# Optimization experiments

Measured on AMD Instinct MI355X. Metric: run time of the kernel, lower is better.

## Reference

```python
import jax, jax.numpy as jnp
import numpy as np


def setup_inputs() -> dict:
    key = jax.random.key(0)
    k1, k2 = jax.random.split(key)
    N, P, SMK, L = 256, 64, 2048, 32
    inp = jax.random.normal(k1, (N, P, SMK, 2), dtype=jnp.float32)
    # channel taps; in the original these are randn scaled by sqrt(power/2)
    cof = jax.random.normal(k2, (N, P, L, 2), dtype=jnp.float32) * 0.1
    return {"input": inp, "cof": cof, "M": 64}


def reference(input, cof, M):
    # input: (N, P, SMK, 2) real/imag stacked; cof: (N, P, L, 2)
    N, P, SMK, _ = input.shape
    L = cof.shape[2]
    sig = (input[..., 0] + 1j * input[..., 1]).reshape(N * P, SMK)   # complex64
    h = (cof[..., 0] + 1j * cof[..., 1]).reshape(N * P, L)
    # torch path: conv1d with time-reversed taps and padding=L-1 == FULL linear
    # convolution; four real convs == one complex conv.
    out_c = jax.vmap(lambda s, k: jnp.convolve(s, k, mode="full"))(sig, h)  # (N*P, SMK+L-1)
    output = jnp.stack([out_c.real, out_c.imag], axis=-1).reshape(N, P, SMK + L - 1, 2)
    # H_t = FFT of zero-padded taps along the tap axis (length M)
    cof_zp = jnp.pad(cof, ((0, 0), (0, 0), (0, M - L), (0, 0)))
    Hc = jnp.fft.fft(cof_zp[..., 0] + 1j * cof_zp[..., 1], axis=-1)  # (N, P, M)
    H_t = jnp.stack([Hc.real, Hc.imag], axis=-1)                      # (N, P, M, 2)
    return output, H_t
```

## Files before the change

kernel.cpp:

```cpp
#include <hip/hip_runtime.h>
#include <math.h>

#define SMK    2048
#define TAPS   32
#define OUTLEN (SMK + TAPS - 1)
#define PAD    32
#define SLOTS  (PAD + SMK + PAD)
#define NF4    (SLOTS / 2)
#define MDFT   64

typedef float v2f __attribute__((ext_vector_type(2)));

__device__ __forceinline__ float rfl(float x) {
    return __int_as_float(__builtin_amdgcn_readfirstlane(__float_as_int(x)));
}

__global__ __launch_bounds__(256, 8)
void conv_kernel(const float* __restrict__ input,
                 const float* __restrict__ cof,
                 float* __restrict__ out0,
                 float* __restrict__ out1)
{
    __shared__ float4 S4[NF4];
    __shared__ float2 s_tw[MDFT];

    const int tid = threadIdx.x;
    const int row = blockIdx.x;

    const float4* gin = (const float4*)(input + (size_t)row * (SMK * 2));
    #pragma unroll
    for (int k = 0; k < 4; ++k) S4[16 + tid + 256 * k] = gin[tid + 256 * k];
    if (tid < 16) {
        S4[tid] = make_float4(0.f, 0.f, 0.f, 0.f);
    } else if (tid < 32) {
        S4[1024 + tid] = make_float4(0.f, 0.f, 0.f, 0.f);
    }
    if (tid >= 64 && tid < 128) {
        int j = tid - 64;
        float sv, cv;
        __sincosf(-2.0f * (float)M_PI * (float)j / (float)MDFT, &sv, &cv);
        s_tw[j] = make_float2(cv, sv);
    }

    const float2* __restrict__ ct = (const float2*)(cof + (size_t)row * (TAPS * 2));
    float hre[TAPS], him[TAPS];
    #pragma unroll
    for (int l = 0; l < TAPS; ++l) {
        float2 tv = ct[l];
        hre[l] = rfl(tv.x);
        him[l] = rfl(tv.y);
    }
    __syncthreads();

    float2* go2 = (float2*)(out0 + (size_t)row * (OUTLEN * 2));

    #pragma unroll 1
    for (int j = 0; j < 2; ++j) {
        const int tf = 4 * tid + 1 + 1024 * j;

        v2f accA[4], accB[4];
        #pragma unroll
        for (int k = 0; k < 4; ++k) { accA[k] = (v2f)(0.f); accB[k] = (v2f)(0.f); }

        #pragma unroll
        for (int c = 0; c < 4; ++c) {
            const int base4 = 2 * tid + 512 * j - 4 * c + 13;
            float4 w4[6];
            #pragma unroll
            for (int i = 0; i < 6; ++i) w4[i] = S4[base4 + i];

            #pragma unroll
            for (int lp = 0; lp < 8; ++lp) {
                const int l = 8 * c + lp;
                const v2f hv = { hre[l], him[l] };
                #pragma unroll
                for (int k = 0; k < 4; ++k) {
                    const int q = k - lp + 7;
                    const float sx = (q & 1) ? w4[q >> 1].z : w4[q >> 1].x;
                    const float sy = (q & 1) ? w4[q >> 1].w : w4[q >> 1].y;
                    accA[k] = __builtin_elementwise_fma((v2f){ sx, sx }, hv, accA[k]);
                    accB[k] = __builtin_elementwise_fma((v2f){ sy, sy }, hv, accB[k]);
                }
            }
            __builtin_amdgcn_sched_barrier(0);
        }

        #pragma unroll
        for (int k = 0; k < 4; ++k)
            go2[tf + k] = make_float2(accA[k].x - accB[k].y, accA[k].y + accB[k].x);
    }

    const float2* S2 = (const float2*)S4;

    if (tid < MDFT) {
        const int kk = tid;
        v2f aA = (v2f)(0.f), aB = (v2f)(0.f);
        #pragma unroll
        for (int l = 0; l < TAPS; ++l) {
            const v2f hv = { hre[l], him[l] };
            float2 w = s_tw[(kk * l) & (MDFT - 1)];
            aA = __builtin_elementwise_fma((v2f){ w.x, w.x }, hv, aA);
            aB = __builtin_elementwise_fma((v2f){ w.y, w.y }, hv, aB);
        }
        ((float2*)out1)[(size_t)row * MDFT + kk] =
            make_float2(aA.x - aB.y, aA.y + aB.x);
    }
    else if (tid >= 128 && tid <= 158) {
        const int t = (tid == 158) ? 0 : (2049 + (tid - 128));
        v2f aA = (v2f)(0.f), aB = (v2f)(0.f);
        #pragma unroll
        for (int l = 0; l < TAPS; ++l) {
            const v2f hv = { hre[l], him[l] };
            float2 s = S2[PAD + t - l];
            aA = __builtin_elementwise_fma((v2f){ s.x, s.x }, hv, aA);
            aB = __builtin_elementwise_fma((v2f){ s.y, s.y }, hv, aB);
        }
        go2[t] = make_float2(aA.x - aB.y, aA.y + aB.x);
    }
}

extern "C" void kernel_launch(void* const* d_in, const int* in_sizes, int n_in,
                              void* d_out, int out_size, void* d_ws, size_t ws_size,
                              hipStream_t stream)
{
    const float* input = (const float*)d_in[0];
    const float* cof   = (const float*)d_in[1];

    const int NP = in_sizes[0] / (SMK * 2);

    float* out0 = (float*)d_out;
    float* out1 = out0 + (size_t)NP * OUTLEN * 2;

    conv_kernel<<<NP, 256, 0, stream>>>(input, cof, out0, out1);
}
```

Baseline: 139.7 us.

## Compute 8 outputs per thread in one pass with XOR-swizzled LDS layout

Each thread now produces 8 consecutive outputs in a single pass instead of two passes of 4, so each LDS window of 8 float4 loads serves more FMAs. The real and imaginary products go into one accumulator per output via a pre-rotated tap vector, which removes the final combine step. The shared-memory signal buffer is XOR-swizzled to cut bank conflicts from the strided per-thread float4 reads. In exchange the kernel uses more registers (8 accumulators, 8-float4 window), which may lower occupancy under the 256x8 launch bounds.

After: 148.5 us. +6.3%, slower.

```diff
diff --git a/kernel.cpp b/kernel.cpp
--- a/kernel.cpp
+++ b/kernel.cpp
@@ -10,6 +10,8 @@
 #define MDFT   64
 
 typedef float v2f __attribute__((ext_vector_type(2)));
+
+__device__ __forceinline__ int swz4(int s) { return s ^ ((s >> 3) & 7); }
 
 __device__ __forceinline__ float rfl(float x) {
     return __int_as_float(__builtin_amdgcn_readfirstlane(__float_as_int(x)));
@@ -29,11 +31,12 @@
 
     const float4* gin = (const float4*)(input + (size_t)row * (SMK * 2));
     #pragma unroll
-    for (int k = 0; k < 4; ++k) S4[16 + tid + 256 * k] = gin[tid + 256 * k];
+    for (int k = 0; k < 4; ++k)
+        S4[swz4(16 + tid + 256 * k)] = gin[tid + 256 * k];
     if (tid < 16) {
-        S4[tid] = make_float4(0.f, 0.f, 0.f, 0.f);
+        S4[swz4(tid)] = make_float4(0.f, 0.f, 0.f, 0.f);
     } else if (tid < 32) {
-        S4[1024 + tid] = make_float4(0.f, 0.f, 0.f, 0.f);
+        S4[swz4(1024 + tid)] = make_float4(0.f, 0.f, 0.f, 0.f);
     }
     if (tid >= 64 && tid < 128) {
         int j = tid - 64;
@@ -54,43 +57,39 @@
 
     float2* go2 = (float2*)(out0 + (size_t)row * (OUTLEN * 2));
 
-    #pragma unroll 1
-    for (int j = 0; j < 2; ++j) {
-        const int tf = 4 * tid + 1 + 1024 * j;
+    const int t0 = 8 * tid + 1;
 
-        v2f accA[4], accB[4];
+    v2f acc[8];
+    #pragma unroll
+    for (int k = 0; k < 8; ++k) acc[k] = (v2f)(0.f);
+
+    #pragma unroll
+    for (int c = 0; c < 4; ++c) {
+        const int base4 = 4 * tid + 13 - 4 * c;
+        float4 w4[8];
         #pragma unroll
-        for (int k = 0; k < 4; ++k) { accA[k] = (v2f)(0.f); accB[k] = (v2f)(0.f); }
+        for (int i = 0; i < 8; ++i) w4[i] = S4[swz4(base4 + i)];
 
         #pragma unroll
-        for (int c = 0; c < 4; ++c) {
-            const int base4 = 2 * tid + 512 * j - 4 * c + 13;
-            float4 w4[6];
+        for (int lp = 0; lp < 8; ++lp) {
+            const int l = 8 * c + lp;
+            const v2f hva = {  hre[l], him[l] };
+            const v2f hvb = { -him[l], hre[l] };
             #pragma unroll
-            for (int i = 0; i < 6; ++i) w4[i] = S4[base4 + i];
-
-            #pragma unroll
-            for (int lp = 0; lp < 8; ++lp) {
-                const int l = 8 * c + lp;
-                const v2f hv = { hre[l], him[l] };
-                #pragma unroll
-                for (int k = 0; k < 4; ++k) {
-                    const int q = k - lp + 7;
-                    const float sx = (q & 1) ? w4[q >> 1].z : w4[q >> 1].x;
-                    const float sy = (q & 1) ? w4[q >> 1].w : w4[q >> 1].y;
-                    accA[k] = __builtin_elementwise_fma((v2f){ sx, sx }, hv, accA[k]);
-                    accB[k] = __builtin_elementwise_fma((v2f){ sy, sy }, hv, accB[k]);
-                }
+            for (int k = 0; k < 8; ++k) {
+                const int m = k - lp + 7;
+                const float sx = (m & 1) ? w4[m >> 1].z : w4[m >> 1].x;
+                const float sy = (m & 1) ? w4[m >> 1].w : w4[m >> 1].y;
+                acc[k] = __builtin_elementwise_fma((v2f){ sx, sx }, hva, acc[k]);
+                acc[k] = __builtin_elementwise_fma((v2f){ sy, sy }, hvb, acc[k]);
             }
-            __builtin_amdgcn_sched_barrier(0);
         }
-
-        #pragma unroll
-        for (int k = 0; k < 4; ++k)
-            go2[tf + k] = make_float2(accA[k].x - accB[k].y, accA[k].y + accB[k].x);
+        __builtin_amdgcn_sched_barrier(0);
     }
 
-    const float2* S2 = (const float2*)S4;
+    #pragma unroll
+    for (int k = 0; k < 8; ++k)
+        go2[t0 + k] = make_float2(acc[k].x, acc[k].y);
 
     if (tid < MDFT) {
         const int kk = tid;
@@ -111,9 +110,12 @@
         #pragma unroll
         for (int l = 0; l < TAPS; ++l) {
             const v2f hv = { hre[l], him[l] };
-            float2 s = S2[PAD + t - l];
-            aA = __builtin_elementwise_fma((v2f){ s.x, s.x }, hv, aA);
-            aB = __builtin_elementwise_fma((v2f){ s.y, s.y }, hv, aB);
+            const int p = PAD + t - l;
+            float4 v = S4[swz4(p >> 1)];
+            const float sx = (p & 1) ? v.z : v.x;
+            const float sy = (p & 1) ? v.w : v.y;
+            aA = __builtin_elementwise_fma((v2f){ sx, sx }, hv, aA);
+            aB = __builtin_elementwise_fma((v2f){ sy, sy }, hv, aB);
         }
         go2[t] = make_float2(aA.x - aB.y, aA.y + aB.x);
     }
```
